# Kernel tuning notes

Measured on AMD Instinct MI355X. Metric: run time of the kernel, lower is better.

Reference implementation:

```python
import jax, jax.numpy as jnp
import numpy as np

D_IN = 4096
UNITS = 4096
NNZ = 262144
BATCH = 1024


def setup_inputs() -> dict:
    key = jax.random.key(0)
    k1, k2, k3, k4, k5 = jax.random.split(key, 5)
    x = jax.random.normal(k1, (BATCH, D_IN), dtype=jnp.float32)
    # trainable sparse kernel values (scaled so outputs stay O(1))
    values = jax.random.normal(k2, (NNZ,), dtype=jnp.float32) * (1.0 / np.sqrt(NNZ / UNITS))
    bias = jax.random.normal(k3, (UNITS,), dtype=jnp.float32) * 0.1
    rows = jax.random.randint(k4, (NNZ,), 0, D_IN, dtype=jnp.int32)
    cols = jax.random.randint(k5, (NNZ,), 0, UNITS, dtype=jnp.int32)
    return {"x": x, "values": values, "bias": bias, "rows": rows, "cols": cols}


def reference(x, values, bias, rows, cols):
    # sparse COO matmul: out[b, c] = sum_{k: cols[k]==c} x[b, rows[k]] * values[k]
    # gather rows of x^T -> [nnz, B], scale by values, scatter-add into columns
    contrib = x.T[rows] * values[:, None]                      # [nnz, B]
    out = jax.ops.segment_sum(contrib, cols, num_segments=UNITS).T  # [B, units]
    out = out + bias[None, :]
    return jax.nn.relu(out)
```

## Files before the change

### kernel.cpp

```cpp
#include <hip/hip_runtime.h>
#include <hip/hip_bf16.h>

#define D_IN  4096
#define UNITS 4096
#define NNZ   262144
#define BATCH 1024
#define CAP   256
#define QB    256
#define NQ    4

#define SCAT_BLKS  (NNZ / 256)
#define TRANS_BLKS ((D_IN / 32) * (BATCH / 32))


__global__ __launch_bounds__(256) void prep_kernel(const float* __restrict__ x,
                                                   const int* __restrict__ rows,
                                                   const int* __restrict__ cols,
                                                   const float* __restrict__ values,
                                                   int* __restrict__ counts,
                                                   int2* __restrict__ buckets,
                                                   unsigned short* __restrict__ xT4) {
    __shared__ float tile[32][33];
    int bx = blockIdx.x;
    if (bx < SCAT_BLKS) {
        int k = bx * 256 + threadIdx.x;
        int c = cols[k];
        int pos = atomicAdd(&counts[c], 1);
        if (pos < CAP) {
            int2 e;
            e.x = rows[k];
            e.y = __float_as_int(values[k]);
            buckets[c * CAP + pos] = e;
        }
        return;
    }
    bx -= SCAT_BLKS;
    const int nr = D_IN / 32;
    int r0 = (bx % nr) * 32;
    int b0 = (bx / nr) * 32;
    int tx = threadIdx.x & 31, ty = threadIdx.x >> 5;
    #pragma unroll
    for (int i = 0; i < 32; i += 8)
        tile[ty + i][tx] = x[(size_t)(b0 + ty + i) * D_IN + r0 + tx];
    __syncthreads();
    int q  = b0 >> 8;
    int bq = (b0 & 255) + tx;
    #pragma unroll
    for (int i = 0; i < 32; i += 8) {
        unsigned bits = __float_as_uint(tile[tx][ty + i]);
        unsigned r = (bits + 0x7FFFu + ((bits >> 16) & 1u)) >> 16;
        xT4[((size_t)q * D_IN + (r0 + ty + i)) * QB + bq] = (unsigned short)r;
    }
}


__device__ __forceinline__ void fma8(float* a, uint4 u, float v) {
    a[0] += __uint_as_float(u.x << 16)         * v;
    a[1] += __uint_as_float(u.x & 0xffff0000u) * v;
    a[2] += __uint_as_float(u.y << 16)         * v;
    a[3] += __uint_as_float(u.y & 0xffff0000u) * v;
    a[4] += __uint_as_float(u.z << 16)         * v;
    a[5] += __uint_as_float(u.z & 0xffff0000u) * v;
    a[6] += __uint_as_float(u.w << 16)         * v;
    a[7] += __uint_as_float(u.w & 0xffff0000u) * v;
}

__global__ __launch_bounds__(256) void spmm_kernel(const unsigned short* __restrict__ xT4,
                                                   const int2* __restrict__ buckets,
                                                   const int* __restrict__ counts,
                                                   const float* __restrict__ bias,
                                                   float* __restrict__ out) {
    __shared__ float tile[4][QB];
    const int bx   = blockIdx.x;
    const int q    = bx & 3;
    const int cg   = bx >> 2;
    const int wave = __builtin_amdgcn_readfirstlane(threadIdx.x >> 6);
    const int lane = threadIdx.x & 63;
    const bool hi  = lane >= 32;
    const int c    = (cg << 2) | wave;

    int n = counts[c];
    if (n > CAP) n = CAP;
    const int2* bk = buckets + (size_t)c * CAP;
    const char* bp = (const char*)(xT4 + (size_t)q * D_IN * QB + (lane & 31) * 8);

    float a[8];
    #pragma unroll
    for (int i = 0; i < 8; ++i) a[i] = 0.f;

    int j = 0;
    for (; j + 8 <= n; j += 8) {
        uint4 e01 = *(const uint4*)(bk + j);
        uint4 e23 = *(const uint4*)(bk + j + 2);
        uint4 e45 = *(const uint4*)(bk + j + 4);
        uint4 e67 = *(const uint4*)(bk + j + 6);
        unsigned o0 = (hi ? e01.z : e01.x) * (QB * 2u);
        unsigned o1 = (hi ? e23.z : e23.x) * (QB * 2u);
        unsigned o2 = (hi ? e45.z : e45.x) * (QB * 2u);
        unsigned o3 = (hi ? e67.z : e67.x) * (QB * 2u);
        float v0 = __uint_as_float(hi ? e01.w : e01.y);
        float v1 = __uint_as_float(hi ? e23.w : e23.y);
        float v2 = __uint_as_float(hi ? e45.w : e45.y);
        float v3 = __uint_as_float(hi ? e67.w : e67.y);
        uint4 u0 = *(const uint4*)(bp + o0);
        uint4 u1 = *(const uint4*)(bp + o1);
        uint4 u2 = *(const uint4*)(bp + o2);
        uint4 u3 = *(const uint4*)(bp + o3);
        fma8(a, u0, v0);
        fma8(a, u1, v1);
        fma8(a, u2, v2);
        fma8(a, u3, v3);
    }
    for (; j + 2 <= n; j += 2) {
        uint4 e01 = *(const uint4*)(bk + j);
        unsigned o0 = (hi ? e01.z : e01.x) * (QB * 2u);
        float v0 = __uint_as_float(hi ? e01.w : e01.y);
        uint4 u0 = *(const uint4*)(bp + o0);
        fma8(a, u0, v0);
    }
    if (j < n) {
        int2 e = bk[j];
        float v = hi ? 0.f : __int_as_float(e.y);
        uint4 u = *(const uint4*)(bp + (unsigned)e.x * (QB * 2u));
        fma8(a, u, v);
    }

    #pragma unroll
    for (int i = 0; i < 8; ++i) a[i] += __shfl_xor(a[i], 32, 64);

    float bv = bias[c];
    if (lane < 32) {
        float* dst = &tile[wave][(lane & 31) * 8];
        float4 r0, r1;
        r0.x = fmaxf(a[0] + bv, 0.f); r0.y = fmaxf(a[1] + bv, 0.f);
        r0.z = fmaxf(a[2] + bv, 0.f); r0.w = fmaxf(a[3] + bv, 0.f);
        r1.x = fmaxf(a[4] + bv, 0.f); r1.y = fmaxf(a[5] + bv, 0.f);
        r1.z = fmaxf(a[6] + bv, 0.f); r1.w = fmaxf(a[7] + bv, 0.f);
        *(float4*)dst = r0;
        *(float4*)(dst + 4) = r1;
    }
    __syncthreads();

    int t = threadIdx.x;
    float4 o;
    o.x = tile[0][t];
    o.y = tile[1][t];
    o.z = tile[2][t];
    o.w = tile[3][t];
    *(float4*)(out + (size_t)(q * QB + t) * UNITS + (cg << 2)) = o;
}


extern "C" void kernel_launch(void* const* d_in, const int* in_sizes, int n_in,
                              void* d_out, int out_size, void* d_ws, size_t ws_size,
                              hipStream_t stream) {
    const float* x      = (const float*)d_in[0];
    const float* values = (const float*)d_in[1];
    const float* bias   = (const float*)d_in[2];
    const int*   rows   = (const int*)d_in[3];
    const int*   cols   = (const int*)d_in[4];
    float* out = (float*)d_out;

    char* ws = (char*)d_ws;
    unsigned short* xT4 = (unsigned short*)(ws);
    int2*  buckets = (int2*)(ws + (size_t)8 * 1024 * 1024);
    int*   counts  = (int*)(ws + (size_t)16 * 1024 * 1024);

    hipMemsetAsync(counts, 0, UNITS * sizeof(int), stream);

    prep_kernel<<<SCAT_BLKS + TRANS_BLKS, 256, 0, stream>>>(x, rows, cols, values,
                                                            counts, buckets, xT4);

    spmm_kernel<<<NQ * 1024, 256, 0, stream>>>(xT4, buckets, counts, bias, out);
}
```

Measured before the change: 126.2 us.

## Store transposed x as fp16 and accumulate with v_fma_mix_f32

```diff
diff --git a/kernel.cpp b/kernel.cpp
--- a/kernel.cpp
+++ b/kernel.cpp
@@ -1,5 +1,5 @@
 #include <hip/hip_runtime.h>
-#include <hip/hip_bf16.h>
+#include <hip/hip_fp16.h>
 
 #define D_IN  4096
 #define UNITS 4096
@@ -19,7 +19,7 @@
                                                    const float* __restrict__ values,
                                                    int* __restrict__ counts,
                                                    int2* __restrict__ buckets,
-                                                   unsigned short* __restrict__ xT4) {
+                                                   unsigned int* __restrict__ xT4w) {
     __shared__ float tile[32][33];
     int bx = blockIdx.x;
     if (bx < SCAT_BLKS) {
@@ -43,26 +43,30 @@
     for (int i = 0; i < 32; i += 8)
         tile[ty + i][tx] = x[(size_t)(b0 + ty + i) * D_IN + r0 + tx];
     __syncthreads();
-    int q  = b0 >> 8;
-    int bq = (b0 & 255) + tx;
+    int q   = b0 >> 8;
+    int bq0 = (b0 & 255) >> 1;
+    int pair = threadIdx.x & 15;
+    int rl   = threadIdx.x >> 4;
     #pragma unroll
-    for (int i = 0; i < 32; i += 8) {
-        unsigned bits = __float_as_uint(tile[tx][ty + i]);
-        unsigned r = (bits + 0x7FFFu + ((bits >> 16) & 1u)) >> 16;
-        xT4[((size_t)q * D_IN + (r0 + ty + i)) * QB + bq] = (unsigned short)r;
+    for (int i = 0; i < 32; i += 16) {
+        int r = rl + i;
+        unsigned short h0 = __half_as_ushort(__float2half(tile[2 * pair][r]));
+        unsigned short h1 = __half_as_ushort(__float2half(tile[2 * pair + 1][r]));
+        unsigned w = (unsigned)h0 | ((unsigned)h1 << 16);
+        xT4w[((size_t)(q * D_IN + r0 + r) * QB >> 1) + bq0 + pair] = w;
     }
 }
 
 
-__device__ __forceinline__ void fma8(float* a, uint4 u, float v) {
-    a[0] += __uint_as_float(u.x << 16)         * v;
-    a[1] += __uint_as_float(u.x & 0xffff0000u) * v;
-    a[2] += __uint_as_float(u.y << 16)         * v;
-    a[3] += __uint_as_float(u.y & 0xffff0000u) * v;
-    a[4] += __uint_as_float(u.z << 16)         * v;
-    a[5] += __uint_as_float(u.z & 0xffff0000u) * v;
-    a[6] += __uint_as_float(u.w << 16)         * v;
-    a[7] += __uint_as_float(u.w & 0xffff0000u) * v;
+__device__ __forceinline__ void fmix8(float* a, uint4 u, float v) {
+    asm("v_fma_mix_f32 %0, %1, %2, %0 op_sel_hi:[1,0,0]"              : "+v"(a[0]) : "v"(u.x), "v"(v));
+    asm("v_fma_mix_f32 %0, %1, %2, %0 op_sel:[1,0,0] op_sel_hi:[1,0,0]" : "+v"(a[1]) : "v"(u.x), "v"(v));
+    asm("v_fma_mix_f32 %0, %1, %2, %0 op_sel_hi:[1,0,0]"              : "+v"(a[2]) : "v"(u.y), "v"(v));
+    asm("v_fma_mix_f32 %0, %1, %2, %0 op_sel:[1,0,0] op_sel_hi:[1,0,0]" : "+v"(a[3]) : "v"(u.y), "v"(v));
+    asm("v_fma_mix_f32 %0, %1, %2, %0 op_sel_hi:[1,0,0]"              : "+v"(a[4]) : "v"(u.z), "v"(v));
+    asm("v_fma_mix_f32 %0, %1, %2, %0 op_sel:[1,0,0] op_sel_hi:[1,0,0]" : "+v"(a[5]) : "v"(u.z), "v"(v));
+    asm("v_fma_mix_f32 %0, %1, %2, %0 op_sel_hi:[1,0,0]"              : "+v"(a[6]) : "v"(u.w), "v"(v));
+    asm("v_fma_mix_f32 %0, %1, %2, %0 op_sel:[1,0,0] op_sel_hi:[1,0,0]" : "+v"(a[7]) : "v"(u.w), "v"(v));
 }
 
 __global__ __launch_bounds__(256) void spmm_kernel(const unsigned short* __restrict__ xT4,
@@ -73,16 +77,17 @@
     __shared__ float tile[4][QB];
     const int bx   = blockIdx.x;
     const int q    = bx & 3;
-    const int cg   = bx >> 2;
+    const int cg   = ((bx >> 3) & 3) | (((bx >> 2) & 1) << 2) | ((bx >> 5) << 3);
     const int wave = __builtin_amdgcn_readfirstlane(threadIdx.x >> 6);
     const int lane = threadIdx.x & 63;
-    const bool hi  = lane >= 32;
+    const int hi01 = lane >> 5;
     const int c    = (cg << 2) | wave;
 
     int n = counts[c];
     if (n > CAP) n = CAP;
-    const int2* bk = buckets + (size_t)c * CAP;
-    const char* bp = (const char*)(xT4 + (size_t)q * D_IN * QB + (lane & 31) * 8);
+    const int2* bk  = buckets + (size_t)c * CAP;
+    const int2* bkl = bk + hi01;
+    const char* bp  = (const char*)(xT4 + (size_t)q * D_IN * QB + (lane & 31) * 8);
 
     float a[8];
     #pragma unroll
@@ -90,39 +95,33 @@
 
     int j = 0;
     for (; j + 8 <= n; j += 8) {
-        uint4 e01 = *(const uint4*)(bk + j);
-        uint4 e23 = *(const uint4*)(bk + j + 2);
-        uint4 e45 = *(const uint4*)(bk + j + 4);
-        uint4 e67 = *(const uint4*)(bk + j + 6);
-        unsigned o0 = (hi ? e01.z : e01.x) * (QB * 2u);
-        unsigned o1 = (hi ? e23.z : e23.x) * (QB * 2u);
-        unsigned o2 = (hi ? e45.z : e45.x) * (QB * 2u);
-        unsigned o3 = (hi ? e67.z : e67.x) * (QB * 2u);
-        float v0 = __uint_as_float(hi ? e01.w : e01.y);
-        float v1 = __uint_as_float(hi ? e23.w : e23.y);
-        float v2 = __uint_as_float(hi ? e45.w : e45.y);
-        float v3 = __uint_as_float(hi ? e67.w : e67.y);
+        int2 e0 = bkl[j];
+        int2 e1 = bkl[j + 2];
+        int2 e2 = bkl[j + 4];
+        int2 e3 = bkl[j + 6];
+        unsigned o0 = (unsigned)e0.x << 9;
+        unsigned o1 = (unsigned)e1.x << 9;
+        unsigned o2 = (unsigned)e2.x << 9;
+        unsigned o3 = (unsigned)e3.x << 9;
         uint4 u0 = *(const uint4*)(bp + o0);
         uint4 u1 = *(const uint4*)(bp + o1);
         uint4 u2 = *(const uint4*)(bp + o2);
         uint4 u3 = *(const uint4*)(bp + o3);
-        fma8(a, u0, v0);
-        fma8(a, u1, v1);
-        fma8(a, u2, v2);
-        fma8(a, u3, v3);
+        fmix8(a, u0, __int_as_float(e0.y));
+        fmix8(a, u1, __int_as_float(e1.y));
+        fmix8(a, u2, __int_as_float(e2.y));
+        fmix8(a, u3, __int_as_float(e3.y));
     }
     for (; j + 2 <= n; j += 2) {
-        uint4 e01 = *(const uint4*)(bk + j);
-        unsigned o0 = (hi ? e01.z : e01.x) * (QB * 2u);
-        float v0 = __uint_as_float(hi ? e01.w : e01.y);
-        uint4 u0 = *(const uint4*)(bp + o0);
-        fma8(a, u0, v0);
+        int2 e = bkl[j];
+        uint4 u = *(const uint4*)(bp + ((unsigned)e.x << 9));
+        fmix8(a, u, __int_as_float(e.y));
     }
     if (j < n) {
         int2 e = bk[j];
-        float v = hi ? 0.f : __int_as_float(e.y);
-        uint4 u = *(const uint4*)(bp + (unsigned)e.x * (QB * 2u));
-        fma8(a, u, v);
+        float v = hi01 ? 0.f : __int_as_float(e.y);
+        uint4 u = *(const uint4*)(bp + ((unsigned)e.x << 9));
+        fmix8(a, u, v);
     }
 
     #pragma unroll
@@ -169,7 +168,7 @@
     hipMemsetAsync(counts, 0, UNITS * sizeof(int), stream);
 
     prep_kernel<<<SCAT_BLKS + TRANS_BLKS, 256, 0, stream>>>(x, rows, cols, values,
-                                                            counts, buckets, xT4);
+                                                            counts, buckets, (unsigned int*)xT4);
 
     spmm_kernel<<<NQ * 1024, 256, 0, stream>>>(xT4, buckets, counts, bias, out);
 }
```

Result: slower. 137.8 us (+9.2%).
